# Kernel optimization log

Hardware: AMD Instinct MI355X
Metric: run time of the kernel (lower is better)

Reference implementation:

```python
import jax, jax.numpy as jnp
import numpy as np

N_NODES = 50000
N_EDGES = 800000
D = 64
H = 128


def setup_inputs() -> dict:
    key = jax.random.key(0)
    ks = jax.random.split(key, 6)
    x = jax.random.normal(ks[0], (N_NODES, D), dtype=jnp.float32)
    edge_index = jax.random.randint(ks[1], (2, N_EDGES), 0, N_NODES, dtype=jnp.int64)
    # GIN MLP params (Linear(D->H) -> ReLU -> Linear(H->D))
    W1 = jax.random.normal(ks[2], (D, H), dtype=jnp.float32) * (1.0 / np.sqrt(D))
    b1 = jnp.zeros((H,), dtype=jnp.float32)
    W2 = jax.random.normal(ks[3], (H, D), dtype=jnp.float32) * (1.0 / np.sqrt(H))
    b2 = jnp.zeros((D,), dtype=jnp.float32)
    eps = jnp.zeros((1, 1), dtype=jnp.float32)  # trainable eps parameter
    return {"x": x, "W1": W1, "b1": b1, "W2": W2, "b2": b2, "eps": eps,
            "edge_index": edge_index}


def reference(x, W1, b1, W2, b2, eps, edge_index):
    src, dst = edge_index[0], edge_index[1]
    # node -> edge gather (0th-order ptensor on each edge = sum of endpoint feats)
    msg = x[src] + x[dst]                                    # [E, D]
    # edge -> node gather: each node sums messages of its incident edges
    agg = (jax.ops.segment_sum(msg, src, num_segments=N_NODES)
           + jax.ops.segment_sum(msg, dst, num_segments=N_NODES))  # [N, D]
    ones = jnp.ones((N_EDGES,), dtype=x.dtype)
    deg = (jax.ops.segment_sum(ones, src, num_segments=N_NODES)
           + jax.ops.segment_sum(ones, dst, num_segments=N_NODES))  # [N]
    # subtract deg*x so aggregation reduces to the plain neighbor sum (GIN)
    neighbor = agg - x * deg[:, None]
    out = (1.0 + eps) * x + neighbor                          # eps is [1,1], broadcasts
    # GIN MLP
    h = jax.nn.relu(out @ W1 + b1)
    return h @ W2 + b2
```

## Files before the change

kernel.cpp:

```cpp
#include <hip/hip_runtime.h>


#define D 64
#define H 128
#define MPW 8
#define REGSH 6
#define REGSZ 64
#define P1_BLOCKS 256
#define EVBUF_SZ 6400
#define NR_MAX 1024
#define NCAP 96
#define PSTR 68

typedef __attribute__((ext_vector_type(8))) short short8;
typedef __attribute__((ext_vector_type(4))) float float4v;

__device__ __forceinline__ float lane_bcast(float v, int l) {
    return __uint_as_float(__builtin_amdgcn_readlane(__float_as_uint(v), l));
}

__device__ __forceinline__ unsigned short f2bf(float f) {
    unsigned int u = __float_as_uint(f);
    u = (u + (((u >> 16) & 1u) + 0x7fffu)) >> 16;
    return (unsigned short)u;
}

__device__ __forceinline__ void bf2_acc(unsigned int u, float& a, float& b) {
    a += __uint_as_float(u << 16);
    b += __uint_as_float(u & 0xffff0000u);
}

__global__ void zero_int_kernel(int* __restrict__ p, int n) {
    int i = blockIdx.x * blockDim.x + threadIdx.x;
    if (i < n) p[i] = 0;
}

__global__ void zero_f_kernel(float* __restrict__ p, int n) {
    int i = blockIdx.x * blockDim.x + threadIdx.x;
    if (i < n) p[i] = 0.0f;
}

__global__ void prep_kernel(unsigned int* __restrict__ xh2, int npairs,
                            int* __restrict__ cursor, int NR, int CAPB,
                            const float* __restrict__ W1,
                            const float* __restrict__ W2,
                            unsigned short* __restrict__ wsW1,
                            unsigned short* __restrict__ wsW2) {
    int i = blockIdx.x * blockDim.x + threadIdx.x;
    if (i < NR) cursor[i] = i * CAPB;
    if (i < 32) xh2[npairs + i] = 0;
    if (i < 8192) {
        int j = i & 7, ln = (i >> 3) & 63;
        int q = (ln >> 4) & 3;
        int tt1 = (i >> 9) & 7, s1 = i >> 12;
        wsW1[i] = f2bf(W1[(s1 * 32 + q * 8 + j) * H + tt1 * 16 + (ln & 15)]);
        int tt2 = (i >> 9) & 3, s2 = i >> 11;
        wsW2[i] = f2bf(W2[(s2 * 32 + q * 8 + j) * D + tt2 * 16 + (ln & 15)]);
    }
}

__global__ __launch_bounds__(256) void part1_kernel(
    const int* __restrict__ src, const int* __restrict__ dst,
    int* __restrict__ cursor, unsigned int* __restrict__ evarr,
    const float* __restrict__ x, unsigned int* __restrict__ xh2, int npairs,
    int E, int N, int NR, int CAPB, int EPB)
{
    __shared__ unsigned int evbuf[EVBUF_SZ];
    __shared__ unsigned int sortbuf[EVBUF_SZ];
    __shared__ unsigned short tickbuf[EVBUF_SZ];
    __shared__ int hist[NR_MAX];
    __shared__ int lbase[NR_MAX];
    __shared__ int gbase[NR_MAX];
    __shared__ int scanw[256];
    int t = threadIdx.x;

    int gstride = gridDim.x * 256;
    for (int i = blockIdx.x * 256 + t; i < npairs; i += gstride) {
        float2 v = *(const float2*)(x + (size_t)i * 2);
        unsigned int a = __float_as_uint(v.x);
        unsigned int b = __float_as_uint(v.y);
        a = (a + (((a >> 16) & 1u) + 0x7fffu)) >> 16;
        b = (b + (((b >> 16) & 1u) + 0x7fffu)) >> 16;
        xh2[i] = a | (b << 16);
    }

    for (int b = t; b < NR; b += 256) hist[b] = 0;
    __syncthreads();

    int e0 = blockIdx.x * EPB;
    int ne = E - e0; if (ne > EPB) ne = EPB; if (ne < 0) ne = 0;
    for (int i = t; i < ne; i += 256) {
        int s = src[e0 + i], d = dst[e0 + i];
        s = (s < 0) ? 0 : ((s >= N) ? N - 1 : s);
        d = (d < 0) ? 0 : ((d >= N) ? N - 1 : d);
        unsigned int ev0 = ((unsigned int)s << 16) | (unsigned int)d;
        unsigned int ev1 = ((unsigned int)d << 16) | (unsigned int)s;
        int k0 = atomicAdd(&hist[s >> REGSH], 1);
        int k1 = atomicAdd(&hist[d >> REGSH], 1);
        evbuf[2 * i]     = ev0; tickbuf[2 * i]     = (unsigned short)k0;
        evbuf[2 * i + 1] = ev1; tickbuf[2 * i + 1] = (unsigned short)k1;
    }
    __syncthreads();

    {
        int i0 = t * 4;
        int h0 = (i0 + 0 < NR) ? hist[i0 + 0] : 0;
        int h1 = (i0 + 1 < NR) ? hist[i0 + 1] : 0;
        int h2 = (i0 + 2 < NR) ? hist[i0 + 2] : 0;
        int h3 = (i0 + 3 < NR) ? hist[i0 + 3] : 0;
        int s4 = h0 + h1 + h2 + h3;
        scanw[t] = s4;
        __syncthreads();
        for (int off = 1; off < 256; off <<= 1) {
            int u = (t >= off) ? scanw[t - off] : 0;
            __syncthreads();
            scanw[t] += u;
            __syncthreads();
        }
        int run = scanw[t] - s4;
        if (i0 + 0 < NR) { lbase[i0 + 0] = run; run += h0; }
        if (i0 + 1 < NR) { lbase[i0 + 1] = run; run += h1; }
        if (i0 + 2 < NR) { lbase[i0 + 2] = run; run += h2; }
        if (i0 + 3 < NR) { lbase[i0 + 3] = run; run += h3; }
    }

    for (int b = t; b < NR; b += 256) {
        int c = hist[b];
        gbase[b] = c ? atomicAdd(&cursor[b], c) : 0;
    }
    __syncthreads();

    int nev = 2 * ne;
    for (int i = t; i < nev; i += 256) {
        unsigned int ev = evbuf[i];
        int reg = (int)(ev >> (16 + REGSH));
        sortbuf[lbase[reg] + (int)tickbuf[i]] = ev;
    }
    __syncthreads();

    for (int i = t; i < nev; i += 256) {
        unsigned int ev = sortbuf[i];
        int reg = (int)(ev >> (16 + REGSH));
        int addr = gbase[reg] + (i - lbase[reg]);
        if (addr < (reg + 1) * CAPB) evarr[addr] = ev;
    }
}

__global__ __launch_bounds__(512) void part2_fused(
    const unsigned int* __restrict__ evarr, const int* __restrict__ cursor,
    const unsigned short* __restrict__ xh, const float* __restrict__ x,
    const float* __restrict__ epsp,
    const unsigned short* __restrict__ wsW1,
    const unsigned short* __restrict__ wsW2,
    const float* __restrict__ b1, const float* __restrict__ b2,
    float* __restrict__ y, int N, int CAPB)
{
    __shared__ unsigned short nbuf[REGSZ * NCAP + 32];
    __shared__ int scnt[REGSZ];
    __shared__ float pre_lds[REGSZ * PSTR];
    __shared__ unsigned short sW1[8192];
    __shared__ unsigned short sW2[8192];
    __shared__ unsigned short hbuf[4 * 16 * H];
    int t = threadIdx.x;
    int b = blockIdx.x;
    if (t < REGSZ) scnt[t] = 0;
#pragma unroll
    for (int i = 0; i < 2; ++i) {
        ((uint4*)sW1)[t + i * 512] = ((const uint4*)wsW1)[t + i * 512];
        ((uint4*)sW2)[t + i * 512] = ((const uint4*)wsW2)[t + i * 512];
    }
    __syncthreads();

    int base = b * CAPB;
    int count = cursor[b] - base;
    if (count < 0) count = 0;
    if (count > CAPB) count = CAPB;

    for (int i = t; i < count; i += 512) {
        unsigned int ev = evarr[base + i];
        int row = (int)((ev >> 16) & (REGSZ - 1));
        int k = atomicAdd(&scnt[row], 1);
        if (k < NCAP) nbuf[row * NCAP + k] = (unsigned short)(ev & 0xffffu);
    }
    __syncthreads();

    int wave = t >> 6, lane = t & 63;
    int r = lane >> 5;
    int h = lane & 31;
    float e1 = 1.0f + epsp[0];

    for (int k = 0; k < 8; ++k) {
        int n = wave * 8 + k;
        int v = b * REGSZ + n;
        int m = (v < N) ? scnt[n] : 0;
        m = (m > NCAP) ? NCAP : m;
        float f0 = 0.0f, f1 = 0.0f;
        for (int j = 0; j < m; j += 32) {
            int cc[16];
#pragma unroll
            for (int q = 0; q < 16; ++q) {
                int ii = j + 2 * q + r;
                int c = (int)nbuf[n * NCAP + ii];
                cc[q] = (ii < m) ? c : N;
            }
            unsigned int u[16];
#pragma unroll
            for (int q = 0; q < 16; ++q)
                u[q] = *(const unsigned int*)(xh + (size_t)cc[q] * D + 2 * h);
#pragma unroll
            for (int q = 0; q < 16; ++q) bf2_acc(u[q], f0, f1);
        }
        f0 += __shfl_xor(f0, 32, 64);
        f1 += __shfl_xor(f1, 32, 64);
        if (r == 0) {
            float2 sv = make_float2(0.0f, 0.0f);
            if (v < N) sv = *(const float2*)(x + (size_t)v * D + 2 * h);
            pre_lds[n * PSTR + 2 * h]     = f0 + e1 * sv.x;
            pre_lds[n * PSTR + 2 * h + 1] = f1 + e1 * sv.y;
        }
    }
    __syncthreads();

    int p = wave >> 1, hh = wave & 1;
    int quad = lane >> 4, lm = lane & 15;
    int row0 = p * 16 + lm;

    short8 a1[2];
#pragma unroll
    for (int s = 0; s < 2; ++s) {
        const float* rp = &pre_lds[row0 * PSTR + s * 32 + quad * 8];
        float4v p0 = *(const float4v*)rp;
        float4v p1 = *(const float4v*)(rp + 4);
        short8 a;
        a[0] = (short)f2bf(p0[0]); a[1] = (short)f2bf(p0[1]);
        a[2] = (short)f2bf(p0[2]); a[3] = (short)f2bf(p0[3]);
        a[4] = (short)f2bf(p1[0]); a[5] = (short)f2bf(p1[1]);
        a[6] = (short)f2bf(p1[2]); a[7] = (short)f2bf(p1[3]);
        a1[s] = a;
    }

    float4v acc1[4];
#pragma unroll
    for (int i = 0; i < 4; ++i) {
        int tt = hh * 4 + i;
        float bb = b1[tt * 16 + lm];
        float4v c = {bb, bb, bb, bb};
#pragma unroll
        for (int s = 0; s < 2; ++s) {
            short8 bw = *(const short8*)&sW1[((s * 8 + tt) * 64 + lane) * 8];
            c = __builtin_amdgcn_mfma_f32_16x16x32_bf16(a1[s], bw, c, 0, 0, 0);
        }
        acc1[i] = c;
    }

    unsigned short* hb = &hbuf[p * 16 * H];
#pragma unroll
    for (int i = 0; i < 4; ++i) {
        int tt = hh * 4 + i;
#pragma unroll
        for (int rr = 0; rr < 4; ++rr) {
            float hv = fmaxf(acc1[i][rr], 0.0f);
            hb[(quad * 4 + rr) * H + tt * 16 + lm] = f2bf(hv);
        }
    }
    __syncthreads();

    short8 a2[4];
#pragma unroll
    for (int s = 0; s < 4; ++s)
        a2[s] = *(const short8*)&hb[lm * H + s * 32 + quad * 8];

    int v0t = b * REGSZ + p * 16;
#pragma unroll
    for (int i = 0; i < 2; ++i) {
        int tt = hh * 2 + i;
        float bb = b2[tt * 16 + lm];
        float4v c = {bb, bb, bb, bb};
#pragma unroll
        for (int s = 0; s < 4; ++s) {
            short8 bw = *(const short8*)&sW2[((s * 4 + tt) * 64 + lane) * 8];
            c = __builtin_amdgcn_mfma_f32_16x16x32_bf16(a2[s], bw, c, 0, 0, 0);
        }
#pragma unroll
        for (int rr = 0; rr < 4; ++rr) {
            int v = v0t + quad * 4 + rr;
            if (v < N) y[(size_t)v * D + tt * 16 + lm] = c[rr];
        }
    }
}


__global__ void count_kernel(const int* __restrict__ ei, int* __restrict__ deg,
                             int twoE, int N) {
    int i = blockIdx.x * blockDim.x + threadIdx.x;
    if (i < twoE) {
        int v = ei[i];
        v = (v < 0) ? 0 : ((v >= N) ? N - 1 : v);
        atomicAdd(&deg[v], 1);
    }
}

__global__ __launch_bounds__(256) void scan_part1(const int* __restrict__ deg,
                                                  int* __restrict__ bsum, int n) {
    __shared__ int red[256];
    int t = threadIdx.x;
    int i = blockIdx.x * 256 + t;
    red[t] = (i < n) ? deg[i] : 0;
    __syncthreads();
    for (int off = 128; off > 0; off >>= 1) {
        if (t < off) red[t] += red[t + off];
        __syncthreads();
    }
    if (t == 0) bsum[blockIdx.x] = red[0];
}

__global__ __launch_bounds__(256) void scan_part2(const int* __restrict__ bsum,
                                                  int* __restrict__ boff,
                                                  int* __restrict__ rowstart_n, int nb) {
    __shared__ int s[256];
    int t = threadIdx.x;
    int v = (t < nb) ? bsum[t] : 0;
    s[t] = v;
    __syncthreads();
    for (int off = 1; off < 256; off <<= 1) {
        int u = (t >= off) ? s[t - off] : 0;
        __syncthreads();
        s[t] += u;
        __syncthreads();
    }
    if (t < nb) boff[t] = s[t] - v;
    if (t == 255) *rowstart_n = s[255];
}

__global__ __launch_bounds__(256) void scan_part3(const int* __restrict__ deg,
                                                  const int* __restrict__ boff,
                                                  int* __restrict__ rowstart,
                                                  int* __restrict__ cursor, int n) {
    __shared__ int s[256];
    int t = threadIdx.x;
    int i = blockIdx.x * 256 + t;
    int v = (i < n) ? deg[i] : 0;
    s[t] = v;
    __syncthreads();
    for (int off = 1; off < 256; off <<= 1) {
        int u = (t >= off) ? s[t - off] : 0;
        __syncthreads();
        s[t] += u;
        __syncthreads();
    }
    if (i < n) {
        int r = boff[blockIdx.x] + s[t] - v;
        rowstart[i] = r;
        cursor[i] = r;
    }
}

__global__ __launch_bounds__(256) void scan_single(const int* __restrict__ deg,
                                                   int* __restrict__ rowstart,
                                                   int* __restrict__ cursor,
                                                   int n, int chunk) {
    __shared__ int psum[256];
    int t = threadIdx.x;
    int lo = t * chunk;
    int hi = lo + chunk; if (hi > n) hi = n;
    int s = 0;
    for (int i = lo; i < hi; ++i) s += deg[i];
    psum[t] = s;
    __syncthreads();
    for (int off = 1; off < 256; off <<= 1) {
        int v = (t >= off) ? psum[t - off] : 0;
        __syncthreads();
        psum[t] += v;
        __syncthreads();
    }
    int run = (t == 0) ? 0 : psum[t - 1];
    for (int i = lo; i < hi; ++i) {
        int d = deg[i];
        rowstart[i] = run;
        cursor[i] = run;
        run += d;
    }
    if (t == 255) rowstart[n] = psum[255];
}

__global__ __launch_bounds__(256) void fill_xcd(
    const int* __restrict__ src, const int* __restrict__ dst,
    int* __restrict__ cursor, int* __restrict__ col,
    int E, int N, int npg)
{
    int grp = blockIdx.x & 7;
    int slice = blockIdx.x >> 3;
    int lo = grp * npg;
    int hi = lo + npg; if (hi > N) hi = N;
    int stride = (gridDim.x >> 3) * 256;
    for (int i = slice * 256 + threadIdx.x; i < E; i += stride) {
        int s = src[i], d = dst[i];
        s = (s < 0) ? 0 : ((s >= N) ? N - 1 : s);
        d = (d < 0) ? 0 : ((d >= N) ? N - 1 : d);
        if (s >= lo && s < hi) { int p = atomicAdd(&cursor[s], 1); col[p] = d; }
        if (d >= lo && d < hi) { int q = atomicAdd(&cursor[d], 1); col[q] = s; }
    }
}

__global__ __launch_bounds__(256) void gather_csr2(
    const float* __restrict__ x, const float* __restrict__ epsp,
    const int* __restrict__ rowstart, const int* __restrict__ col,
    float* __restrict__ pre, int N)
{
    int wid = (blockIdx.x * 256 + threadIdx.x) >> 6;
    int lane = threadIdx.x & 63;
    int v0 = wid * 2;
    if (v0 >= N) return;
    int v1 = v0 + 1;
    float eps1 = 1.0f + epsp[0];
    int j0 = rowstart[v0], re0 = rowstart[v0 + 1];
    float a0 = eps1 * x[(size_t)v0 * D + lane];
    int j1 = 0, re1 = 0;
    float a1 = 0.0f;
    if (v1 < N) {
        j1 = rowstart[v1]; re1 = rowstart[v1 + 1];
        a1 = eps1 * x[(size_t)v1 * D + lane];
    }
    while (j0 + 8 <= re0 && j1 + 8 <= re1) {
        float p0 = x[(size_t)col[j0 + 0] * D + lane];
        float p1 = x[(size_t)col[j0 + 1] * D + lane];
        float p2 = x[(size_t)col[j0 + 2] * D + lane];
        float p3 = x[(size_t)col[j0 + 3] * D + lane];
        float p4 = x[(size_t)col[j0 + 4] * D + lane];
        float p5 = x[(size_t)col[j0 + 5] * D + lane];
        float p6 = x[(size_t)col[j0 + 6] * D + lane];
        float p7 = x[(size_t)col[j0 + 7] * D + lane];
        float q0 = x[(size_t)col[j1 + 0] * D + lane];
        float q1 = x[(size_t)col[j1 + 1] * D + lane];
        float q2 = x[(size_t)col[j1 + 2] * D + lane];
        float q3 = x[(size_t)col[j1 + 3] * D + lane];
        float q4 = x[(size_t)col[j1 + 4] * D + lane];
        float q5 = x[(size_t)col[j1 + 5] * D + lane];
        float q6 = x[(size_t)col[j1 + 6] * D + lane];
        float q7 = x[(size_t)col[j1 + 7] * D + lane];
        a0 += ((p0 + p1) + (p2 + p3)) + ((p4 + p5) + (p6 + p7));
        a1 += ((q0 + q1) + (q2 + q3)) + ((q4 + q5) + (q6 + q7));
        j0 += 8; j1 += 8;
    }
    for (; j0 + 8 <= re0; j0 += 8) {
        float p0 = x[(size_t)col[j0 + 0] * D + lane];
        float p1 = x[(size_t)col[j0 + 1] * D + lane];
        float p2 = x[(size_t)col[j0 + 2] * D + lane];
        float p3 = x[(size_t)col[j0 + 3] * D + lane];
        float p4 = x[(size_t)col[j0 + 4] * D + lane];
        float p5 = x[(size_t)col[j0 + 5] * D + lane];
        float p6 = x[(size_t)col[j0 + 6] * D + lane];
        float p7 = x[(size_t)col[j0 + 7] * D + lane];
        a0 += ((p0 + p1) + (p2 + p3)) + ((p4 + p5) + (p6 + p7));
    }
    for (; j1 + 8 <= re1; j1 += 8) {
        float q0 = x[(size_t)col[j1 + 0] * D + lane];
        float q1 = x[(size_t)col[j1 + 1] * D + lane];
        float q2 = x[(size_t)col[j1 + 2] * D + lane];
        float q3 = x[(size_t)col[j1 + 3] * D + lane];
        float q4 = x[(size_t)col[j1 + 4] * D + lane];
        float q5 = x[(size_t)col[j1 + 5] * D + lane];
        float q6 = x[(size_t)col[j1 + 6] * D + lane];
        float q7 = x[(size_t)col[j1 + 7] * D + lane];
        a1 += ((q0 + q1) + (q2 + q3)) + ((q4 + q5) + (q6 + q7));
    }
    for (; j0 < re0; ++j0) a0 += x[(size_t)col[j0] * D + lane];
    for (; j1 < re1; ++j1) a1 += x[(size_t)col[j1] * D + lane];
    pre[(size_t)v0 * D + lane] = a0;
    if (v1 < N) pre[(size_t)v1 * D + lane] = a1;
}

__device__ __forceinline__ void mlp_store(
    const float* acc, float* sW, int v0, int t, int lane, int nNodes,
    const float* __restrict__ W2,
    const float* __restrict__ b1, const float* __restrict__ b2,
    float* __restrict__ y)
{
    float b1a = b1[lane], b1b = b1[lane + 64];
    float ha[MPW], hb[MPW];
#pragma unroll
    for (int m = 0; m < MPW; ++m) { ha[m] = b1a; hb[m] = b1b; }
#pragma unroll 4
    for (int f = 0; f < D; ++f) {
        float wa = sW[f * H + lane];
        float wb = sW[f * H + lane + 64];
#pragma unroll
        for (int m = 0; m < MPW; ++m) {
            float o = lane_bcast(acc[m], f);
            ha[m] += o * wa;
            hb[m] += o * wb;
        }
    }
#pragma unroll
    for (int m = 0; m < MPW; ++m) {
        ha[m] = fmaxf(ha[m], 0.0f);
        hb[m] = fmaxf(hb[m], 0.0f);
    }

    __syncthreads();
    for (int i = t; i < H * D; i += 256) sW[i] = W2[i];
    __syncthreads();

    float b2v = b2[lane];
    float yv[MPW];
#pragma unroll
    for (int m = 0; m < MPW; ++m) yv[m] = b2v;
#pragma unroll 4
    for (int k = 0; k < 64; ++k) {
        float w = sW[k * D + lane];
#pragma unroll
        for (int m = 0; m < MPW; ++m) yv[m] += lane_bcast(ha[m], k) * w;
    }
#pragma unroll 4
    for (int k = 0; k < 64; ++k) {
        float w = sW[(k + 64) * D + lane];
#pragma unroll
        for (int m = 0; m < MPW; ++m) yv[m] += lane_bcast(hb[m], k) * w;
    }
#pragma unroll
    for (int m = 0; m < MPW; ++m) {
        int v = v0 + m;
        if (v < nNodes) y[(size_t)v * D + lane] = yv[m];
    }
}

__global__ __launch_bounds__(256) void mlp_pre(
    const float* __restrict__ pre, const float* __restrict__ W1,
    const float* __restrict__ b1, const float* __restrict__ W2,
    const float* __restrict__ b2, float* __restrict__ y, int nNodes)
{
    __shared__ float sW[D * H];
    int t = threadIdx.x;
    for (int i = t; i < D * H; i += 256) sW[i] = W1[i];
    __syncthreads();
    int wave = t >> 6, lane = t & 63;
    int v0 = (blockIdx.x * 4 + wave) * MPW;
    float acc[MPW];
#pragma unroll
    for (int m = 0; m < MPW; ++m) {
        int v = v0 + m;
        acc[m] = (v < nNodes) ? pre[(size_t)v * D + lane] : 0.0f;
    }
    mlp_store(acc, sW, v0, t, lane, nNodes, W2, b1, b2, y);
}

__global__ __launch_bounds__(256) void gather_mlp_csr(
    const float* __restrict__ x, const float* __restrict__ W1,
    const float* __restrict__ b1, const float* __restrict__ W2,
    const float* __restrict__ b2, const float* __restrict__ epsp,
    const int* __restrict__ rowstart, const int* __restrict__ col,
    float* __restrict__ y, int nNodes)
{
    __shared__ float sW[D * H];
    int t = threadIdx.x;
    for (int i = t; i < D * H; i += 256) sW[i] = W1[i];
    __syncthreads();
    int wave = t >> 6, lane = t & 63;
    float eps1 = 1.0f + epsp[0];
    int v0 = (blockIdx.x * 4 + wave) * MPW;
    float acc[MPW];
#pragma unroll
    for (int m = 0; m < MPW; ++m) {
        int v = v0 + m;
        float a = 0.0f;
        if (v < nNodes) {
            int rs = rowstart[v], re = rowstart[v + 1];
            a = eps1 * x[(size_t)v * D + lane];
            int j = rs;
            for (; j + 8 <= re; j += 8) {
                float p0 = x[(size_t)col[j + 0] * D + lane];
                float p1 = x[(size_t)col[j + 1] * D + lane];
                float p2 = x[(size_t)col[j + 2] * D + lane];
                float p3 = x[(size_t)col[j + 3] * D + lane];
                float p4 = x[(size_t)col[j + 4] * D + lane];
                float p5 = x[(size_t)col[j + 5] * D + lane];
                float p6 = x[(size_t)col[j + 6] * D + lane];
                float p7 = x[(size_t)col[j + 7] * D + lane];
                a += ((p0 + p1) + (p2 + p3)) + ((p4 + p5) + (p6 + p7));
            }
            for (; j < re; ++j) a += x[(size_t)col[j] * D + lane];
        }
        acc[m] = a;
    }
    mlp_store(acc, sW, v0, t, lane, nNodes, W2, b1, b2, y);
}

__global__ void scatter_kernel(const float* __restrict__ x,
                               const int* __restrict__ src,
                               const int* __restrict__ dst,
                               float* __restrict__ agg, int E, int N)
{
    int tid = blockIdx.x * blockDim.x + threadIdx.x;
    int e = tid >> 6, lane = tid & 63;
    if (e < E) {
        int s = src[e], d = dst[e];
        s = (s < 0) ? 0 : ((s >= N) ? N - 1 : s);
        d = (d < 0) ? 0 : ((d >= N) ? N - 1 : d);
        float xs = x[(size_t)s * D + lane];
        float xd = x[(size_t)d * D + lane];
        atomicAdd(&agg[(size_t)s * D + lane], xd);
        atomicAdd(&agg[(size_t)d * D + lane], xs);
    }
}

__global__ __launch_bounds__(256) void mlp_from_agg(
    const float* __restrict__ x, const float* __restrict__ W1,
    const float* __restrict__ b1, const float* __restrict__ W2,
    const float* __restrict__ b2, const float* __restrict__ epsp,
    float* __restrict__ yio, int nNodes)
{
    __shared__ float sW[D * H];
    int t = threadIdx.x;
    for (int i = t; i < D * H; i += 256) sW[i] = W1[i];
    __syncthreads();
    int wave = t >> 6, lane = t & 63;
    float eps1 = 1.0f + epsp[0];
    int v0 = (blockIdx.x * 4 + wave) * MPW;
    float acc[MPW];
#pragma unroll
    for (int m = 0; m < MPW; ++m) {
        int v = v0 + m;
        acc[m] = (v < nNodes)
                   ? (eps1 * x[(size_t)v * D + lane] + yio[(size_t)v * D + lane])
                   : 0.0f;
    }
    mlp_store(acc, sW, v0, t, lane, nNodes, W2, b1, b2, yio);
}

extern "C" void kernel_launch(void* const* d_in, const int* in_sizes, int n_in,
                              void* d_out, int out_size, void* d_ws, size_t ws_size,
                              hipStream_t stream)
{
    const float* x   = (const float*)d_in[0];
    const float* W1  = (const float*)d_in[1];
    const float* b1  = (const float*)d_in[2];
    const float* W2  = (const float*)d_in[3];
    const float* b2  = (const float*)d_in[4];
    const float* eps = (const float*)d_in[5];
    const int*   ei  = (const int*)d_in[6];
    float* out = (float*)d_out;

    int N = in_sizes[0] / D;
    int E = in_sizes[6] / 2;
    const int* src = ei;
    const int* dst = ei + E;

    int nb = (N + 255) / 256;

    int NR = (N + REGSZ - 1) >> REGSH;
    int meanE = (NR > 0) ? (2 * E + NR - 1) / NR : 0;
    int CAPB = meanE + meanE / 4 + 128;
    int EPB = (E + P1_BLOCKS - 1) / P1_BLOCKS;
    size_t off_cur  = 0;
    size_t off_ev   = (off_cur + (size_t)NR * 4 + 15) & ~(size_t)15;
    size_t off_xh   = (off_ev + (size_t)NR * CAPB * 4 + 15) & ~(size_t)15;
    size_t off_w1   = (off_xh + (size_t)(N + 1) * D * 2 + 15) & ~(size_t)15;
    size_t off_w2   = off_w1 + 8192 * 2;
    size_t need_part = off_w2 + 8192 * 2;

    size_t csr_ints = (size_t)(3 * N + 1 + 2 * E) + 512;
    size_t need_csr = csr_ints * sizeof(int);
    size_t need_split = need_csr + (size_t)N * D * sizeof(float);
    int mlp_blocks = (N + 4 * MPW - 1) / (4 * MPW);

    if (ws_size >= need_part && N >= REGSZ && N <= 65535
        && NR <= NR_MAX && 2 * EPB <= EVBUF_SZ && (N * D) % 2 == 0) {
        char* base = (char*)d_ws;
        int*            cursor = (int*)(base + off_cur);
        unsigned int*   evarr  = (unsigned int*)(base + off_ev);
        unsigned short* xh     = (unsigned short*)(base + off_xh);
        unsigned short* wsW1   = (unsigned short*)(base + off_w1);
        unsigned short* wsW2   = (unsigned short*)(base + off_w2);
        int npairs = N * D / 2;

        prep_kernel<<<32, 256, 0, stream>>>(
            (unsigned int*)xh, npairs, cursor, NR, CAPB, W1, W2, wsW1, wsW2);
        part1_kernel<<<P1_BLOCKS, 256, 0, stream>>>(
            src, dst, cursor, evarr, x, (unsigned int*)xh, npairs,
            E, N, NR, CAPB, EPB);
        part2_fused<<<NR, 512, 0, stream>>>(
            evarr, cursor, xh, x, eps, wsW1, wsW2, b1, b2, out, N, CAPB);
    } else if (ws_size >= need_csr) {
        int*   deg      = (int*)d_ws;
        int*   cursor   = deg + N;
        int*   rowstart = cursor + N;
        int*   col      = rowstart + (N + 1);
        int*   bsum     = col + 2 * E;
        int*   boff     = bsum + 256;
        float* pre      = (float*)(boff + 256);

        zero_int_kernel<<<(N + 255) / 256, 256, 0, stream>>>(deg, N);
        count_kernel<<<(2 * E + 255) / 256, 256, 0, stream>>>(ei, deg, 2 * E, N);
        if (nb <= 256) {
            scan_part1<<<nb, 256, 0, stream>>>(deg, bsum, N);
            scan_part2<<<1, 256, 0, stream>>>(bsum, boff, &rowstart[N], nb);
            scan_part3<<<nb, 256, 0, stream>>>(deg, boff, rowstart, cursor, N);
        } else {
            int chunk = (N + 255) / 256;
            scan_single<<<1, 256, 0, stream>>>(deg, rowstart, cursor, N, chunk);
        }
        fill_xcd<<<2048, 256, 0, stream>>>(src, dst, cursor, col, E, N, (N + 7) / 8);
        int waves = (N + 1) / 2;
        int gather_blocks = (waves + 3) / 4;
        if (ws_size >= need_split) {
            gather_csr2<<<gather_blocks, 256, 0, stream>>>(x, eps, rowstart, col, pre, N);
            mlp_pre<<<mlp_blocks, 256, 0, stream>>>(pre, W1, b1, W2, b2, out, N);
        } else {
            gather_mlp_csr<<<mlp_blocks, 256, 0, stream>>>(
                x, W1, b1, W2, b2, eps, rowstart, col, out, N);
        }
    } else {
        int nd = N * D;
        zero_f_kernel<<<(nd + 255) / 256, 256, 0, stream>>>(out, nd);
        long long st = (long long)E * 64;
        scatter_kernel<<<(int)((st + 255) / 256), 256, 0, stream>>>(x, src, dst, out, E, N);
        mlp_from_agg<<<mlp_blocks, 256, 0, stream>>>(x, W1, b1, W2, b2, eps, out, N);
    }
}
```

Before: 146.8 us.

## Split bf16 node features into two feature-half tables for cache-friendlier gathers

The packed bf16 copy of x becomes two separate tables, each holding 32 features per node. The neighbor-gather loop now makes two passes, one per half, and each wave handles two nodes at once with 16-lane groups reading 64-byte rows. Each pass touches a 3.2MB table instead of one 6.4MB table, so the gathers should hit L2 more often. The cost is twice the neighbor-index reads, extra shuffle reductions, and lanes left idle when two paired nodes have different degrees.

Measured after the change: 159.6 us. 1.09x slower.

```diff
diff --git a/kernel.cpp b/kernel.cpp
--- a/kernel.cpp
+++ b/kernel.cpp
@@ -40,7 +40,8 @@
     if (i < n) p[i] = 0.0f;
 }
 
-__global__ void prep_kernel(unsigned int* __restrict__ xh2, int npairs,
+__global__ void prep_kernel(unsigned int* __restrict__ xt0,
+                            unsigned int* __restrict__ xt1, int N,
                             int* __restrict__ cursor, int NR, int CAPB,
                             const float* __restrict__ W1,
                             const float* __restrict__ W2,
@@ -48,7 +49,10 @@
                             unsigned short* __restrict__ wsW2) {
     int i = blockIdx.x * blockDim.x + threadIdx.x;
     if (i < NR) cursor[i] = i * CAPB;
-    if (i < 32) xh2[npairs + i] = 0;
+    if (i < 16) {
+        xt0[(size_t)N * 16 + i] = 0;
+        xt1[(size_t)N * 16 + i] = 0;
+    }
     if (i < 8192) {
         int j = i & 7, ln = (i >> 3) & 63;
         int q = (ln >> 4) & 3;
@@ -62,8 +66,9 @@
 __global__ __launch_bounds__(256) void part1_kernel(
     const int* __restrict__ src, const int* __restrict__ dst,
     int* __restrict__ cursor, unsigned int* __restrict__ evarr,
-    const float* __restrict__ x, unsigned int* __restrict__ xh2, int npairs,
-    int E, int N, int NR, int CAPB, int EPB)
+    const float* __restrict__ x,
+    unsigned int* __restrict__ xt0, unsigned int* __restrict__ xt1,
+    int npairs, int E, int N, int NR, int CAPB, int EPB)
 {
     __shared__ unsigned int evbuf[EVBUF_SZ];
     __shared__ unsigned int sortbuf[EVBUF_SZ];
@@ -81,7 +86,10 @@
         unsigned int b = __float_as_uint(v.y);
         a = (a + (((a >> 16) & 1u) + 0x7fffu)) >> 16;
         b = (b + (((b >> 16) & 1u) + 0x7fffu)) >> 16;
-        xh2[i] = a | (b << 16);
+        unsigned int w = a | (b << 16);
+        int vv = i >> 5, p = i & 31;
+        if (p < 16) xt0[(size_t)vv * 16 + p] = w;
+        else        xt1[(size_t)vv * 16 + (p - 16)] = w;
     }
 
     for (int b = t; b < NR; b += 256) hist[b] = 0;
@@ -148,8 +156,8 @@
 
 __global__ __launch_bounds__(512) void part2_fused(
     const unsigned int* __restrict__ evarr, const int* __restrict__ cursor,
-    const unsigned short* __restrict__ xh, const float* __restrict__ x,
-    const float* __restrict__ epsp,
+    const unsigned short* __restrict__ xh0, const unsigned short* __restrict__ xh1,
+    const float* __restrict__ x, const float* __restrict__ epsp,
     const unsigned short* __restrict__ wsW1,
     const unsigned short* __restrict__ wsW2,
     const float* __restrict__ b1, const float* __restrict__ b2,
@@ -185,38 +193,61 @@
     __syncthreads();
 
     int wave = t >> 6, lane = t & 63;
-    int r = lane >> 5;
-    int h = lane & 31;
+    int r4 = lane >> 4;
+    int h16 = lane & 15;
     float e1 = 1.0f + epsp[0];
 
-    for (int k = 0; k < 8; ++k) {
-        int n = wave * 8 + k;
-        int v = b * REGSZ + n;
-        int m = (v < N) ? scnt[n] : 0;
-        m = (m > NCAP) ? NCAP : m;
-        float f0 = 0.0f, f1 = 0.0f;
-        for (int j = 0; j < m; j += 32) {
-            int cc[16];
-#pragma unroll
-            for (int q = 0; q < 16; ++q) {
-                int ii = j + 2 * q + r;
-                int c = (int)nbuf[n * NCAP + ii];
-                cc[q] = (ii < m) ? c : N;
+#pragma unroll
+    for (int fh = 0; fh < 2; ++fh) {
+        const unsigned short* xt = fh ? xh1 : xh0;
+        for (int kk = 0; kk < 8; kk += 2) {
+            int n0 = wave * 8 + kk, n1 = n0 + 1;
+            int v0 = b * REGSZ + n0, v1 = v0 + 1;
+            int m0 = (v0 < N) ? scnt[n0] : 0; m0 = (m0 > NCAP) ? NCAP : m0;
+            int m1 = (v1 < N) ? scnt[n1] : 0; m1 = (m1 > NCAP) ? NCAP : m1;
+            int mmax = (m0 > m1) ? m0 : m1;
+            float a0 = 0.0f, a1 = 0.0f;
+            float c0 = 0.0f, c1 = 0.0f;
+            for (int j = 0; j < mmax; j += 32) {
+                int cc[16];
+#pragma unroll
+                for (int q = 0; q < 8; ++q) {
+                    int ii = j + 4 * q + r4;
+                    int c = (int)nbuf[n0 * NCAP + ii];
+                    cc[q] = (ii < m0) ? c : N;
+                }
+#pragma unroll
+                for (int q = 0; q < 8; ++q) {
+                    int ii = j + 4 * q + r4;
+                    int c = (int)nbuf[n1 * NCAP + ii];
+                    cc[8 + q] = (ii < m1) ? c : N;
+                }
+                unsigned int u[16];
+#pragma unroll
+                for (int q = 0; q < 16; ++q)
+                    u[q] = *(const unsigned int*)(xt + (size_t)cc[q] * 32 + 2 * h16);
+#pragma unroll
+                for (int q = 0; q < 8; ++q) bf2_acc(u[q], a0, a1);
+#pragma unroll
+                for (int q = 8; q < 16; ++q) bf2_acc(u[q], c0, c1);
             }
-            unsigned int u[16];
-#pragma unroll
-            for (int q = 0; q < 16; ++q)
-                u[q] = *(const unsigned int*)(xh + (size_t)cc[q] * D + 2 * h);
-#pragma unroll
-            for (int q = 0; q < 16; ++q) bf2_acc(u[q], f0, f1);
-        }
-        f0 += __shfl_xor(f0, 32, 64);
-        f1 += __shfl_xor(f1, 32, 64);
-        if (r == 0) {
-            float2 sv = make_float2(0.0f, 0.0f);
-            if (v < N) sv = *(const float2*)(x + (size_t)v * D + 2 * h);
-            pre_lds[n * PSTR + 2 * h]     = f0 + e1 * sv.x;
-            pre_lds[n * PSTR + 2 * h + 1] = f1 + e1 * sv.y;
+            a0 += __shfl_xor(a0, 16, 64); a0 += __shfl_xor(a0, 32, 64);
+            a1 += __shfl_xor(a1, 16, 64); a1 += __shfl_xor(a1, 32, 64);
+            c0 += __shfl_xor(c0, 16, 64); c0 += __shfl_xor(c0, 32, 64);
+            c1 += __shfl_xor(c1, 16, 64); c1 += __shfl_xor(c1, 32, 64);
+            if (r4 == 0) {
+                float2 sv = make_float2(0.0f, 0.0f);
+                if (v0 < N)
+                    sv = *(const float2*)(x + (size_t)v0 * D + fh * 32 + 2 * h16);
+                pre_lds[n0 * PSTR + fh * 32 + 2 * h16]     = a0 + e1 * sv.x;
+                pre_lds[n0 * PSTR + fh * 32 + 2 * h16 + 1] = a1 + e1 * sv.y;
+            } else if (r4 == 1) {
+                float2 sv = make_float2(0.0f, 0.0f);
+                if (v1 < N)
+                    sv = *(const float2*)(x + (size_t)v1 * D + fh * 32 + 2 * h16);
+                pre_lds[n1 * PSTR + fh * 32 + 2 * h16]     = c0 + e1 * sv.x;
+                pre_lds[n1 * PSTR + fh * 32 + 2 * h16 + 1] = c1 + e1 * sv.y;
+            }
         }
     }
     __syncthreads();
@@ -225,7 +256,7 @@
     int quad = lane >> 4, lm = lane & 15;
     int row0 = p * 16 + lm;
 
-    short8 a1[2];
+    short8 a1f[2];
 #pragma unroll
     for (int s = 0; s < 2; ++s) {
         const float* rp = &pre_lds[row0 * PSTR + s * 32 + quad * 8];
@@ -236,7 +267,7 @@
         a[2] = (short)f2bf(p0[2]); a[3] = (short)f2bf(p0[3]);
         a[4] = (short)f2bf(p1[0]); a[5] = (short)f2bf(p1[1]);
         a[6] = (short)f2bf(p1[2]); a[7] = (short)f2bf(p1[3]);
-        a1[s] = a;
+        a1f[s] = a;
     }
 
     float4v acc1[4];
@@ -248,7 +279,7 @@
 #pragma unroll
         for (int s = 0; s < 2; ++s) {
             short8 bw = *(const short8*)&sW1[((s * 8 + tt) * 64 + lane) * 8];
-            c = __builtin_amdgcn_mfma_f32_16x16x32_bf16(a1[s], bw, c, 0, 0, 0);
+            c = __builtin_amdgcn_mfma_f32_16x16x32_bf16(a1f[s], bw, c, 0, 0, 0);
         }
         acc1[i] = c;
     }
@@ -653,8 +684,9 @@
     int EPB = (E + P1_BLOCKS - 1) / P1_BLOCKS;
     size_t off_cur  = 0;
     size_t off_ev   = (off_cur + (size_t)NR * 4 + 15) & ~(size_t)15;
-    size_t off_xh   = (off_ev + (size_t)NR * CAPB * 4 + 15) & ~(size_t)15;
-    size_t off_w1   = (off_xh + (size_t)(N + 1) * D * 2 + 15) & ~(size_t)15;
+    size_t off_xh0  = (off_ev + (size_t)NR * CAPB * 4 + 15) & ~(size_t)15;
+    size_t off_xh1  = (off_xh0 + (size_t)(N + 1) * 32 * 2 + 15) & ~(size_t)15;
+    size_t off_w1   = (off_xh1 + (size_t)(N + 1) * 32 * 2 + 15) & ~(size_t)15;
     size_t off_w2   = off_w1 + 8192 * 2;
     size_t need_part = off_w2 + 8192 * 2;
 
@@ -668,18 +700,21 @@
         char* base = (char*)d_ws;
         int*            cursor = (int*)(base + off_cur);
         unsigned int*   evarr  = (unsigned int*)(base + off_ev);
-        unsigned short* xh     = (unsigned short*)(base + off_xh);
+        unsigned short* xh0    = (unsigned short*)(base + off_xh0);
+        unsigned short* xh1    = (unsigned short*)(base + off_xh1);
         unsigned short* wsW1   = (unsigned short*)(base + off_w1);
         unsigned short* wsW2   = (unsigned short*)(base + off_w2);
         int npairs = N * D / 2;
 
         prep_kernel<<<32, 256, 0, stream>>>(
-            (unsigned int*)xh, npairs, cursor, NR, CAPB, W1, W2, wsW1, wsW2);
+            (unsigned int*)xh0, (unsigned int*)xh1, N, cursor, NR, CAPB,
+            W1, W2, wsW1, wsW2);
         part1_kernel<<<P1_BLOCKS, 256, 0, stream>>>(
-            src, dst, cursor, evarr, x, (unsigned int*)xh, npairs,
+            src, dst, cursor, evarr, x,
+            (unsigned int*)xh0, (unsigned int*)xh1, npairs,
             E, N, NR, CAPB, EPB);
         part2_fused<<<NR, 512, 0, stream>>>(
-            evarr, cursor, xh, x, eps, wsW1, wsW2, b1, b2, out, N, CAPB);
+            evarr, cursor, xh0, xh1, x, eps, wsW1, wsW2, b1, b2, out, N, CAPB);
     } else if (ws_size >= need_csr) {
         int*   deg      = (int*)d_ws;
         int*   cursor   = deg + N;
```
